# Kernel tuning notes

Measured on AMD Instinct MI355X. Metric: run time of the kernel, lower is better.

## Reference

```python
import jax, jax.numpy as jnp
import numpy as np

PI = np.pi


def _rot(axis, a):
    c, s = jnp.cos(a), jnp.sin(a)
    o, z = jnp.ones_like(a), jnp.zeros_like(a)
    if axis == 'X':
        flat = (o, z, z, z, c, -s, z, s, c)
    elif axis == 'Y':
        flat = (c, z, s, z, o, z, -s, z, c)
    else:  # 'Z'
        flat = (c, -s, z, s, c, z, z, z, o)
    return jnp.stack(flat, -1).reshape(3, 3)


def setup_inputs() -> dict:
    key = jax.random.key(0)
    k1, k2 = jax.random.split(key)
    H, W = 1080, 1920
    # world points: spread ~50 around origin, camera at z=100 looking back
    PntCld = jax.random.normal(k1, (400000, 3), dtype=jnp.float32) * 50.0
    # detected corners in pixel coordinates
    dtcCor = jax.random.uniform(k2, (128, 2), dtype=jnp.float32) * jnp.array([W, H], jnp.float32)
    cam_pos = jnp.array([0.0, 0.0, 100.0], jnp.float32)
    theta = jnp.array([5.0, -3.0, 10.0], jnp.float32)  # degrees
    view_angle = jnp.array([60.0], jnp.float32)        # degrees
    return {"PntCld": PntCld, "dtcCor": dtcCor, "cam_pos": cam_pos,
            "theta": theta, "view_angle": view_angle, "height": H, "width": W}


def reference(PntCld, dtcCor, cam_pos, theta, view_angle, height, width):
    th = theta * (PI / 180.0)
    R = _rot('Z', th[2]) @ (_rot('Y', th[1]) @ _rot('X', th[0]))  # (3,3)
    f = -height / (2.0 * jnp.tan(view_angle[0] / 2.0 * (PI / 180.0)))
    K = jnp.stack([f, 0.0, width / 2 - 0.5,
                   0.0, f, height / 2 - 0.5,
                   0.0, 0.0, 1.0]).reshape(3, 3)
    translated = PntCld - cam_pos                 # (N_p,3)
    xyz = translated @ R.T                        # rotate each point
    xyz_prime = xyz / xyz[:, 2:3]                 # perspective divide
    uv = xyz_prime @ K.T                          # (N_p,3) pixel coords
    # y-invert and shift by image height, keep (u,v)
    uv_final = jnp.stack([uv[:, 0], height - uv[:, 1]], -1)  # (N_p,2)
    # pairwise squared distances via ||a||^2 + ||b||^2 - 2 a.b (no (N_d,N_p,2) tensor)
    d2 = (jnp.sum(dtcCor ** 2, -1)[:, None]
          + jnp.sum(uv_final ** 2, -1)[None, :]
          - 2.0 * dtcCor @ uv_final.T)            # (N_d,N_p)
    return jnp.sum(jnp.min(d2, axis=1))
```

## Files before the change

### kernel.cpp

```cpp
#include <hip/hip_runtime.h>
#include <math.h>

#define TILE  512
#define BLOCK 256
#define NC    128


__global__ __launch_bounds__(BLOCK) void proj_min_kernel(
        const float* __restrict__ pnt,
        const float* __restrict__ cor,
        const float* __restrict__ cam,
        const float* __restrict__ theta,
        const float* __restrict__ vang,
        const int* __restrict__ hh,
        const int* __restrict__ ww,
        float* __restrict__ pbmin,
        int n) {
    __shared__ float4 uvb[TILE];
    __shared__ float red[4 * NC];
    __shared__ float sc[12];

    const int tid  = threadIdx.x;
    const int base = blockIdx.x * TILE;

    const int i0 = base + 2 * tid;
    float p0x = 0.f, p0y = 0.f, p0z = 0.f;
    float p1x = 0.f, p1y = 0.f, p1z = 0.f;
    const bool v0 = (i0 < n), v1 = (i0 + 1 < n);
    if (v1) {
        const float2* q = (const float2*)(pnt + 3 * i0);
        float2 a = q[0], b = q[1], c = q[2];
        p0x = a.x; p0y = a.y; p0z = b.x;
        p1x = b.y; p1y = c.x; p1z = c.y;
    } else if (v0) {
        p0x = pnt[3 * i0]; p0y = pnt[3 * i0 + 1]; p0z = pnt[3 * i0 + 2];
    }

    if (tid == 0) {
        const double D2R = 0.017453292519943295;
        double a = (double)theta[0] * D2R;
        double b = (double)theta[1] * D2R;
        double c = (double)theta[2] * D2R;
        double sa = sin(a), ca = cos(a);
        double sb = sin(b), cb = cos(b);
        double sc_ = sin(c), cc = cos(c);
        double H = (double)hh[0], W = (double)ww[0];
        double fd = -H / (2.0 * tan((double)vang[0] * 0.5 * D2R));
        sc[0] = (float)(cc * cb);
        sc[1] = (float)(cc * sb * sa - sc_ * ca);
        sc[2] = (float)(cc * sb * ca + sc_ * sa);
        sc[3] = (float)(sc_ * cb);
        sc[4] = (float)(sc_ * sb * sa + cc * ca);
        sc[5] = (float)(sc_ * sb * ca - cc * sa);
        sc[6] = (float)(-sb);
        sc[7] = (float)(cb * sa);
        sc[8] = (float)(cb * ca);
        sc[9]  = (float)fd;
        sc[10] = (float)(W * 0.5 - 0.5);
        sc[11] = (float)(H * 0.5 + 0.5);
    }
    __syncthreads();

    const float r00 = sc[0], r01 = sc[1], r02 = sc[2];
    const float r10 = sc[3], r11 = sc[4], r12 = sc[5];
    const float r20 = sc[6], r21 = sc[7], r22 = sc[8];
    const float f = sc[9], cx = sc[10], cyv = sc[11];
    const float c0 = cam[0], c1 = cam[1], c2 = cam[2];

    {
        float u0 = 0.f, w0 = 0.f, b20 = 3.0e38f;
        float u1 = 0.f, w1 = 0.f, b21 = 3.0e38f;
        if (v0) {
            float tx = p0x - c0, ty = p0y - c1, tz = p0z - c2;
            float x = fmaf(r00, tx, fmaf(r01, ty, r02 * tz));
            float y = fmaf(r10, tx, fmaf(r11, ty, r12 * tz));
            float z = fmaf(r20, tx, fmaf(r21, ty, r22 * tz));
            float xz = x / z, yz = y / z;
            u0 = fmaf(f, xz, cx);
            w0 = fmaf(-f, yz, cyv);
            b20 = fmaf(u0, u0, w0 * w0);
        }
        if (v1) {
            float tx = p1x - c0, ty = p1y - c1, tz = p1z - c2;
            float x = fmaf(r00, tx, fmaf(r01, ty, r02 * tz));
            float y = fmaf(r10, tx, fmaf(r11, ty, r12 * tz));
            float z = fmaf(r20, tx, fmaf(r21, ty, r22 * tz));
            float xz = x / z, yz = y / z;
            u1 = fmaf(f, xz, cx);
            w1 = fmaf(-f, yz, cyv);
            b21 = fmaf(u1, u1, w1 * w1);
        }
        uvb[2 * tid]     = make_float4(u0, w0, b20, 0.f);
        uvb[2 * tid + 1] = make_float4(u1, w1, b21, 0.f);
    }
    __syncthreads();

    const int lane = tid & 63;
    const int w    = tid >> 6;
    const int h    = lane >> 5;
    const int sl   = lane & 31;
    const int cb   = sl << 2;

    float bx[4], by[4], m[4];
    #pragma unroll
    for (int k = 0; k < 4; ++k) {
        bx[k] = -2.f * cor[2 * (cb + k)];
        by[k] = -2.f * cor[2 * (cb + k) + 1];
        m[k]  = 3.4e38f;
    }

    const float4* p = &uvb[(w << 7) + (h << 6)];
    #pragma unroll 8
    for (int j = 0; j < 64; ++j) {
        float4 q = p[j];
        #pragma unroll
        for (int k = 0; k < 4; ++k)
            m[k] = fminf(m[k], fmaf(bx[k], q.x, fmaf(by[k], q.y, q.z)));
    }

    #pragma unroll
    for (int k = 0; k < 4; ++k)
        m[k] = fminf(m[k], __shfl_xor(m[k], 32));
    if (lane < 32) {
        #pragma unroll
        for (int k = 0; k < 4; ++k)
            red[w * NC + cb + k] = m[k];
    }
    __syncthreads();

    if (tid < NC) {
        float mm = fminf(fminf(red[tid], red[NC + tid]),
                         fminf(red[2 * NC + tid], red[3 * NC + tid]));
        pbmin[blockIdx.x * NC + tid] = mm;
    }
}

__global__ __launch_bounds__(64) void colmin_kernel(
        const float* __restrict__ pbmin,
        const float* __restrict__ cor,
        float* __restrict__ stage, int NB) {
    const int c = blockIdx.x;
    const int t = threadIdx.x;
    float m = 3.4e38f;
    for (int r = t; r < NB; r += 64)
        m = fminf(m, pbmin[r * NC + c]);
    #pragma unroll
    for (int off = 32; off > 0; off >>= 1)
        m = fminf(m, __shfl_down(m, off));
    if (t == 0) {
        float ax = cor[2 * c], ay = cor[2 * c + 1];
        stage[c] = m + fmaf(ax, ax, ay * ay);
    }
}

__global__ void sum_kernel(const float* __restrict__ stage,
                           float* __restrict__ out) {
    const int t = threadIdx.x;
    double s = (double)stage[t] + (double)stage[t + 64];
    #pragma unroll
    for (int off = 32; off > 0; off >>= 1)
        s += __shfl_down(s, off);
    if (t == 0) out[0] = (float)s;
}

extern "C" void kernel_launch(void* const* d_in, const int* in_sizes, int n_in,
                              void* d_out, int out_size, void* d_ws, size_t ws_size,
                              hipStream_t stream) {
    const float* pnt   = (const float*)d_in[0];
    const float* cor   = (const float*)d_in[1];
    const float* cam   = (const float*)d_in[2];
    const float* theta = (const float*)d_in[3];
    const float* vang  = (const float*)d_in[4];
    const int*   hh    = (const int*)d_in[5];
    const int*   ww    = (const int*)d_in[6];

    int n  = in_sizes[0] / 3;
    int NB = (n + TILE - 1) / TILE;

    float* pbmin = (float*)d_ws;
    float* stage = (float*)((char*)d_ws + 448 * 1024);

    proj_min_kernel<<<NB, BLOCK, 0, stream>>>(pnt, cor, cam, theta, vang,
                                              hh, ww, pbmin, n);
    colmin_kernel<<<NC, 64, 0, stream>>>(pbmin, cor, stage, NB);
    sum_kernel<<<1, 64, 0, stream>>>(stage, (float*)d_out);
}
```

Measured before the change: 79.72 us.

## Widen per-thread register tile to 8 corners and fuse final sum via last-block atomics

```diff
diff --git a/kernel.cpp b/kernel.cpp
--- a/kernel.cpp
+++ b/kernel.cpp
@@ -15,13 +15,16 @@
         const int* __restrict__ hh,
         const int* __restrict__ ww,
         float* __restrict__ pbmin,
+        unsigned* __restrict__ done,
         int n) {
-    __shared__ float4 uvb[TILE];
+    __shared__ float uu[TILE], vv[TILE], bb[TILE];
     __shared__ float red[4 * NC];
     __shared__ float sc[12];
 
     const int tid  = threadIdx.x;
     const int base = blockIdx.x * TILE;
+
+    if (blockIdx.x == 0 && tid == 0) *done = 0u;
 
     const int i0 = base + 2 * tid;
     float p0x = 0.f, p0y = 0.f, p0z = 0.f;
@@ -90,41 +93,57 @@
             w1 = fmaf(-f, yz, cyv);
             b21 = fmaf(u1, u1, w1 * w1);
         }
-        uvb[2 * tid]     = make_float4(u0, w0, b20, 0.f);
-        uvb[2 * tid + 1] = make_float4(u1, w1, b21, 0.f);
+        *(float2*)(uu + 2 * tid) = make_float2(u0, u1);
+        *(float2*)(vv + 2 * tid) = make_float2(w0, w1);
+        *(float2*)(bb + 2 * tid) = make_float2(b20, b21);
     }
     __syncthreads();
 
     const int lane = tid & 63;
     const int w    = tid >> 6;
-    const int h    = lane >> 5;
-    const int sl   = lane & 31;
-    const int cb   = sl << 2;
-
-    float bx[4], by[4], m[4];
-    #pragma unroll
-    for (int k = 0; k < 4; ++k) {
+    const int q    = lane >> 4;
+    const int sl   = lane & 15;
+    const int cb   = sl << 3;
+
+    float bx[8], by[8], m[8];
+    #pragma unroll
+    for (int k = 0; k < 8; ++k) {
         bx[k] = -2.f * cor[2 * (cb + k)];
         by[k] = -2.f * cor[2 * (cb + k) + 1];
         m[k]  = 3.4e38f;
     }
 
-    const float4* p = &uvb[(w << 7) + (h << 6)];
-    #pragma unroll 8
-    for (int j = 0; j < 64; ++j) {
-        float4 q = p[j];
+    const float4* uu4 = (const float4*)uu;
+    const float4* vv4 = (const float4*)vv;
+    const float4* bb4 = (const float4*)bb;
+    const int g0 = (w * 4 + q) * 8;
+
+    #pragma unroll
+    for (int j = 0; j < 8; ++j) {
+        const int gi = g0 + ((j + 2 * q) & 7);
+        float4 u4 = uu4[gi];
+        float4 v4 = vv4[gi];
+        float4 b4 = bb4[gi];
         #pragma unroll
-        for (int k = 0; k < 4; ++k)
-            m[k] = fminf(m[k], fmaf(bx[k], q.x, fmaf(by[k], q.y, q.z)));
-    }
-
-    #pragma unroll
-    for (int k = 0; k < 4; ++k)
+        for (int k = 0; k < 8; ++k) {
+            m[k] = fminf(m[k], fmaf(bx[k], u4.x, fmaf(by[k], v4.x, b4.x)));
+            m[k] = fminf(m[k], fmaf(bx[k], u4.y, fmaf(by[k], v4.y, b4.y)));
+            m[k] = fminf(m[k], fmaf(bx[k], u4.z, fmaf(by[k], v4.z, b4.z)));
+            m[k] = fminf(m[k], fmaf(bx[k], u4.w, fmaf(by[k], v4.w, b4.w)));
+        }
+    }
+
+    #pragma unroll
+    for (int k = 0; k < 8; ++k)
+        m[k] = fminf(m[k], __shfl_xor(m[k], 16));
+    #pragma unroll
+    for (int k = 0; k < 8; ++k)
         m[k] = fminf(m[k], __shfl_xor(m[k], 32));
-    if (lane < 32) {
+    if (lane < 16) {
         #pragma unroll
-        for (int k = 0; k < 4; ++k)
-            red[w * NC + cb + k] = m[k];
+        for (int k = 0; k < 8; k += 4)
+            *(float4*)(red + w * NC + cb + k) =
+                make_float4(m[k], m[k + 1], m[k + 2], m[k + 3]);
     }
     __syncthreads();
 
@@ -135,10 +154,12 @@
     }
 }
 
-__global__ __launch_bounds__(64) void colmin_kernel(
+__global__ __launch_bounds__(64) void colmin_sum_kernel(
         const float* __restrict__ pbmin,
         const float* __restrict__ cor,
-        float* __restrict__ stage, int NB) {
+        float* __restrict__ stage,
+        unsigned* __restrict__ done,
+        float* __restrict__ out, int NB) {
     const int c = blockIdx.x;
     const int t = threadIdx.x;
     float m = 3.4e38f;
@@ -147,20 +168,27 @@
     #pragma unroll
     for (int off = 32; off > 0; off >>= 1)
         m = fminf(m, __shfl_down(m, off));
+
+    __shared__ int last;
     if (t == 0) {
         float ax = cor[2 * c], ay = cor[2 * c + 1];
-        stage[c] = m + fmaf(ax, ax, ay * ay);
-    }
-}
-
-__global__ void sum_kernel(const float* __restrict__ stage,
-                           float* __restrict__ out) {
-    const int t = threadIdx.x;
-    double s = (double)stage[t] + (double)stage[t + 64];
-    #pragma unroll
-    for (int off = 32; off > 0; off >>= 1)
-        s += __shfl_down(s, off);
-    if (t == 0) out[0] = (float)s;
+        __hip_atomic_store(&stage[c], m + fmaf(ax, ax, ay * ay),
+                           __ATOMIC_RELEASE, __HIP_MEMORY_SCOPE_AGENT);
+        unsigned old = __hip_atomic_fetch_add(done, 1u, __ATOMIC_ACQ_REL,
+                                              __HIP_MEMORY_SCOPE_AGENT);
+        last = (old == NC - 1) ? 1 : 0;
+    }
+    __syncthreads();
+    if (last) {
+        double s = (double)__hip_atomic_load(&stage[t], __ATOMIC_ACQUIRE,
+                                             __HIP_MEMORY_SCOPE_AGENT)
+                 + (double)__hip_atomic_load(&stage[t + 64], __ATOMIC_ACQUIRE,
+                                             __HIP_MEMORY_SCOPE_AGENT);
+        #pragma unroll
+        for (int off = 32; off > 0; off >>= 1)
+            s += __shfl_down(s, off);
+        if (t == 0) out[0] = (float)s;
+    }
 }
 
 extern "C" void kernel_launch(void* const* d_in, const int* in_sizes, int n_in,
@@ -177,11 +205,12 @@
     int n  = in_sizes[0] / 3;
     int NB = (n + TILE - 1) / TILE;
 
-    float* pbmin = (float*)d_ws;
-    float* stage = (float*)((char*)d_ws + 448 * 1024);
+    float*    pbmin = (float*)d_ws;
+    float*    stage = (float*)((char*)d_ws + 512 * 1024);
+    unsigned* done  = (unsigned*)((char*)d_ws + 516 * 1024);
 
     proj_min_kernel<<<NB, BLOCK, 0, stream>>>(pnt, cor, cam, theta, vang,
-                                              hh, ww, pbmin, n);
-    colmin_kernel<<<NC, 64, 0, stream>>>(pbmin, cor, stage, NB);
-    sum_kernel<<<1, 64, 0, stream>>>(stage, (float*)d_out);
+                                              hh, ww, pbmin, done, n);
+    colmin_sum_kernel<<<NC, 64, 0, stream>>>(pbmin, cor, stage, done,
+                                             (float*)d_out, NB);
 }
```

After: 83.44 us. +4.7%, slower.
